# Performance work log

Measured on AMD Instinct MI355X. Metric: run time of the kernel, lower is better.

The kernel has to match this reference:

```python
import jax, jax.numpy as jnp
import numpy as np

N_NODES = 100000   # total atoms in the batched graph
N_EDGES = 1600000  # bonds (directed), avg degree 16
N_GRAPHS = 2000    # molecules in the batch
D_IN, D_H, D_OUT = 600, 300, 2  # 600 = embedding_dim(150) * 4


def setup_inputs() -> dict:
    key = jax.random.key(0)
    ks = jax.random.split(key, 8)
    node_feats = jax.random.normal(ks[0], (N_NODES, D_IN), dtype=jnp.float32)
    W1 = jax.random.normal(ks[1], (D_IN, D_H), dtype=jnp.float32) * (1.0 / np.sqrt(D_IN))
    b1 = jnp.zeros((D_H,), dtype=jnp.float32)
    W2 = jax.random.normal(ks[2], (D_H, D_H), dtype=jnp.float32) * (1.0 / np.sqrt(D_H))
    b2 = jnp.zeros((D_H,), dtype=jnp.float32)
    Wfc = jax.random.normal(ks[3], (D_H, D_OUT), dtype=jnp.float32) * (1.0 / np.sqrt(D_H))
    bfc = jnp.zeros((D_OUT,), dtype=jnp.float32)
    src = jax.random.randint(ks[4], (N_EDGES,), 0, N_NODES, dtype=jnp.int32).astype(jnp.int64)
    dst = jax.random.randint(ks[5], (N_EDGES,), 0, N_NODES, dtype=jnp.int32).astype(jnp.int64)
    graph_id = jnp.sort(jax.random.randint(ks[6], (N_NODES,), 0, N_GRAPHS, dtype=jnp.int32)).astype(jnp.int64)
    return {"node_feats": node_feats, "W1": W1, "b1": b1, "W2": W2, "b2": b2,
            "Wfc": Wfc, "bfc": bfc, "src": src, "dst": dst, "graph_id": graph_id}


def _gcn_layer(x, W, b, src, dst, inv_sqrt_out, inv_sqrt_in):
    # DGL GraphConv (norm='both'): h_i = d_i^{-1/2} * sum_{j->i} d_j^{-1/2} (x_j W) + b
    # weight applied before aggregation (in_feats >= out_feats path), math identical either way.
    h = x @ W                                  # [N, d_out]
    m = h * inv_sqrt_out[:, None]              # scale by src out-degree^{-1/2}
    agg = jax.ops.segment_sum(m[src], dst, num_segments=N_NODES)  # [N, d_out]
    return agg * inv_sqrt_in[:, None] + b


def reference(node_feats, W1, b1, W2, b2, Wfc, bfc, src, dst, graph_id):
    ones_e = jnp.ones((src.shape[0],), dtype=node_feats.dtype)
    deg_out = jax.ops.segment_sum(ones_e, src, num_segments=N_NODES)
    deg_in = jax.ops.segment_sum(ones_e, dst, num_segments=N_NODES)
    inv_sqrt_out = jnp.where(deg_out > 0, jax.lax.rsqrt(jnp.maximum(deg_out, 1.0)), 0.0)
    inv_sqrt_in = jnp.where(deg_in > 0, jax.lax.rsqrt(jnp.maximum(deg_in, 1.0)), 0.0)

    h = jax.nn.relu(_gcn_layer(node_feats, W1, b1, src, dst, inv_sqrt_out, inv_sqrt_in))
    h = jax.nn.relu(_gcn_layer(h, W2, b2, src, dst, inv_sqrt_out, inv_sqrt_in))
    p = jax.nn.softmax(h @ Wfc + bfc, axis=-1)  # [N, 2] per-node class probs

    # per-graph mean pooling (unbatch + mean over each graph's nodes)
    pooled_sum = jax.ops.segment_sum(p, graph_id, num_segments=N_GRAPHS)
    counts = jax.ops.segment_sum(jnp.ones((N_NODES,), dtype=p.dtype), graph_id, num_segments=N_GRAPHS)
    return pooled_sum / jnp.maximum(counts, 1.0)[:, None]  # [G, 2]
```

## Files before the change

### kernel.cpp

```cpp
#include <hip/hip_runtime.h>
#include <hip/hip_bf16.h>

#define N_NODES 100000
#define N_EDGES 1600000
#define N_GRAPHS 2000
#define D_IN 600
#define D_H 300
#define D_OUT 2

#define NPAD 320
#define K1PAD 640
#define K2PAD 320
#define MPAD 100096

typedef __bf16 bf16;
typedef __bf16 bf16x8 __attribute__((ext_vector_type(8)));
typedef float f32x4 __attribute__((ext_vector_type(4)));

__device__ __forceinline__ void gload16(const void* g, void* l) {
    __builtin_amdgcn_global_load_lds(
        (const __attribute__((address_space(1))) unsigned int*)g,
        (__attribute__((address_space(3))) unsigned int*)l, 16, 0, 0);
}

__global__ __launch_bounds__(256) void count_deg(const int* __restrict__ src,
                                                 const int* __restrict__ dst,
                                                 int* __restrict__ deg_out,
                                                 int* __restrict__ deg_in) {
    int e = blockIdx.x * blockDim.x + threadIdx.x;
    if (e < N_EDGES) {
        atomicAdd(&deg_out[src[e]], 1);
        atomicAdd(&deg_in[dst[e]], 1);
    }
}

__global__ __launch_bounds__(256) void block_sum(const int* __restrict__ deg_in,
                                                 int* __restrict__ bsum) {
    __shared__ int s[256];
    int i = blockIdx.x * 256 + threadIdx.x;
    s[threadIdx.x] = (i < N_NODES) ? deg_in[i] : 0;
    __syncthreads();
    for (int off = 128; off; off >>= 1) {
        if (threadIdx.x < off) s[threadIdx.x] += s[threadIdx.x + off];
        __syncthreads();
    }
    if (threadIdx.x == 0) bsum[blockIdx.x] = s[0];
}

__global__ void scan_serial(const int* __restrict__ bsum, int* __restrict__ boff, int nb) {
    if (threadIdx.x == 0 && blockIdx.x == 0) {
        int run = 0;
        for (int i = 0; i < nb; ++i) { boff[i] = run; run += bsum[i]; }
    }
}

__global__ __launch_bounds__(256) void node_offsets(const int* __restrict__ deg_in,
                                                    const int* __restrict__ deg_out,
                                                    const int* __restrict__ boff,
                                                    int* __restrict__ row_start,
                                                    int* __restrict__ cursor,
                                                    float* __restrict__ inv_in,
                                                    float* __restrict__ inv_out) {
    __shared__ int s[256];
    int i = blockIdx.x * 256 + threadIdx.x;
    int d = (i < N_NODES) ? deg_in[i] : 0;
    s[threadIdx.x] = d;
    __syncthreads();
    for (int off = 1; off < 256; off <<= 1) {
        int v = 0;
        if (threadIdx.x >= off) v = s[threadIdx.x - off];
        __syncthreads();
        if (threadIdx.x >= off) s[threadIdx.x] += v;
        __syncthreads();
    }
    if (i < N_NODES) {
        int excl = s[threadIdx.x] - d;
        int rs = boff[blockIdx.x] + excl;
        row_start[i] = rs;
        cursor[i] = rs;
        int di = deg_in[i];
        int dout = deg_out[i];
        inv_in[i]  = (di   > 0) ? rsqrtf((float)di)   : 0.0f;
        inv_out[i] = (dout > 0) ? rsqrtf((float)dout) : 0.0f;
    }
}

__global__ __launch_bounds__(256) void fill_csr(const int* __restrict__ src,
                                                const int* __restrict__ dst,
                                                int* __restrict__ cursor,
                                                int* __restrict__ adj) {
    int e = blockIdx.x * blockDim.x + threadIdx.x;
    if (e < N_EDGES) {
        int pos = atomicAdd(&cursor[dst[e]], 1);
        adj[pos] = src[e];
    }
}

__global__ __launch_bounds__(256) void conv_x(const float* __restrict__ x, bf16* __restrict__ xb) {
    size_t idx = (size_t)blockIdx.x * 256 + threadIdx.x;
    size_t r = idx / (K1PAD / 8);
    int c8 = (int)(idx % (K1PAD / 8)) * 8;
    if (r >= MPAD) return;
    bf16x8 v = {};
    if (r < N_NODES && c8 < D_IN) {
        const float* p = x + r * D_IN + c8;
        float4 f0 = *(const float4*)p;
        float4 f1 = *(const float4*)(p + 4);
        v[0] = (bf16)f0.x; v[1] = (bf16)f0.y; v[2] = (bf16)f0.z; v[3] = (bf16)f0.w;
        v[4] = (bf16)f1.x; v[5] = (bf16)f1.y; v[6] = (bf16)f1.z; v[7] = (bf16)f1.w;
    }
    *(bf16x8*)(xb + r * K1PAD + c8) = v;
}

__global__ __launch_bounds__(256) void conv_bt(const float* __restrict__ W, bf16* __restrict__ Bt,
                                               int K, int N, int Kpad) {
    int idx = blockIdx.x * 256 + threadIdx.x;
    int k = idx % Kpad;
    int n = idx / Kpad;
    if (n >= NPAD) return;
    bf16 v = (bf16)0.0f;
    if (k < K && n < N) v = (bf16)W[(size_t)k * N + n];
    Bt[(size_t)n * Kpad + k] = v;
}

__global__ __launch_bounds__(256) void prep_small(const float* __restrict__ b1,
                                                  const float* __restrict__ b2,
                                                  const float* __restrict__ Wfc,
                                                  float* __restrict__ b1p,
                                                  float* __restrict__ b2p,
                                                  float* __restrict__ wfcp) {
    int i = blockIdx.x * 256 + threadIdx.x;
    if (i < NPAD) {
        b1p[i] = (i < D_H) ? b1[i] : 0.f;
        b2p[i] = (i < D_H) ? b2[i] : 0.f;
    }
    if (i < NPAD * 2) {
        wfcp[i] = (i < D_H * 2) ? Wfc[i] : 0.f;
    }
}

__global__ __launch_bounds__(512) void mfma_gemm(const bf16* __restrict__ A,
                                                 const bf16* __restrict__ Bt,
                                                 const float* __restrict__ rowscale,
                                                 bf16* __restrict__ C,
                                                 int M, int Kpad) {
    __shared__ bf16 As[128 * 64];
    __shared__ bf16 Bs[320 * 64];
    const int tid = threadIdx.x;
    const int lane = tid & 63;
    const int wid = tid >> 6;
    const int wr = wid >> 2;
    const int wc = wid & 3;
    const int blockRow = blockIdx.x * 128;
    const size_t rowBytes = (size_t)Kpad * 2;

    f32x4 acc[4][5] = {};

    const int nK = Kpad >> 6;
    for (int t = 0; t < nK; ++t) {
        const size_t kByte = (size_t)t * 128;
#pragma unroll
        for (int c = 0; c < 2; ++c) {
            int o = c * 8192 + tid * 16;
            int row = o >> 7;
            int slot = (o >> 4) & 7;
            int srcs = slot ^ (row & 7);
            const char* g = (const char*)A + (size_t)(blockRow + row) * rowBytes + kByte + srcs * 16;
            gload16(g, (char*)As + o);
        }
#pragma unroll
        for (int c = 0; c < 5; ++c) {
            int o = c * 8192 + tid * 16;
            int row = o >> 7;
            int slot = (o >> 4) & 7;
            int srcs = slot ^ (row & 7);
            const char* g = (const char*)Bt + (size_t)row * rowBytes + kByte + srcs * 16;
            gload16(g, (char*)Bs + o);
        }
        __syncthreads();
#pragma unroll
        for (int kk = 0; kk < 2; ++kk) {
            int slot = kk * 4 + (lane >> 4);
            bf16x8 af[4], bfr[5];
#pragma unroll
            for (int mi = 0; mi < 4; ++mi) {
                int row = wr * 64 + mi * 16 + (lane & 15);
                int addr = row * 128 + ((slot ^ (row & 7)) << 4);
                af[mi] = *(const bf16x8*)((const char*)As + addr);
            }
#pragma unroll
            for (int ni = 0; ni < 5; ++ni) {
                int row = wc * 80 + ni * 16 + (lane & 15);
                int addr = row * 128 + ((slot ^ (row & 7)) << 4);
                bfr[ni] = *(const bf16x8*)((const char*)Bs + addr);
            }
#pragma unroll
            for (int mi = 0; mi < 4; ++mi)
#pragma unroll
                for (int ni = 0; ni < 5; ++ni)
                    acc[mi][ni] = __builtin_amdgcn_mfma_f32_16x16x32_bf16(af[mi], bfr[ni], acc[mi][ni], 0, 0, 0);
        }
        __syncthreads();
    }
#pragma unroll
    for (int mi = 0; mi < 4; ++mi) {
#pragma unroll
        for (int i = 0; i < 4; ++i) {
            int gr = blockRow + wr * 64 + mi * 16 + ((lane >> 4) << 2) + i;
            if (gr >= M) continue;
            float sc = rowscale[gr];
#pragma unroll
            for (int ni = 0; ni < 5; ++ni) {
                int gc = wc * 80 + ni * 16 + (lane & 15);
                C[(size_t)gr * NPAD + gc] = (bf16)(acc[mi][ni][i] * sc);
            }
        }
    }
}

__device__ __forceinline__ void gather8(const bf16* __restrict__ m,
                                        const int* __restrict__ adj,
                                        int s, int d, int c, float acc[8]) {
    int e = 0;
    for (; e + 8 <= d; e += 8) {
        bf16x8 v0 = *(const bf16x8*)(m + (size_t)adj[s + e + 0] * NPAD + c);
        bf16x8 v1 = *(const bf16x8*)(m + (size_t)adj[s + e + 1] * NPAD + c);
        bf16x8 v2 = *(const bf16x8*)(m + (size_t)adj[s + e + 2] * NPAD + c);
        bf16x8 v3 = *(const bf16x8*)(m + (size_t)adj[s + e + 3] * NPAD + c);
        bf16x8 v4 = *(const bf16x8*)(m + (size_t)adj[s + e + 4] * NPAD + c);
        bf16x8 v5 = *(const bf16x8*)(m + (size_t)adj[s + e + 5] * NPAD + c);
        bf16x8 v6 = *(const bf16x8*)(m + (size_t)adj[s + e + 6] * NPAD + c);
        bf16x8 v7 = *(const bf16x8*)(m + (size_t)adj[s + e + 7] * NPAD + c);
#pragma unroll
        for (int q = 0; q < 8; ++q)
            acc[q] += ((float)v0[q] + (float)v1[q]) + ((float)v2[q] + (float)v3[q]) +
                      ((float)v4[q] + (float)v5[q]) + ((float)v6[q] + (float)v7[q]);
    }
    if (e + 4 <= d) {
        bf16x8 v0 = *(const bf16x8*)(m + (size_t)adj[s + e + 0] * NPAD + c);
        bf16x8 v1 = *(const bf16x8*)(m + (size_t)adj[s + e + 1] * NPAD + c);
        bf16x8 v2 = *(const bf16x8*)(m + (size_t)adj[s + e + 2] * NPAD + c);
        bf16x8 v3 = *(const bf16x8*)(m + (size_t)adj[s + e + 3] * NPAD + c);
#pragma unroll
        for (int q = 0; q < 8; ++q)
            acc[q] += ((float)v0[q] + (float)v1[q]) + ((float)v2[q] + (float)v3[q]);
        e += 4;
    }
    for (; e < d; ++e) {
        bf16x8 v = *(const bf16x8*)(m + (size_t)adj[s + e] * NPAD + c);
#pragma unroll
        for (int q = 0; q < 8; ++q) acc[q] += (float)v[q];
    }
}

__global__ __launch_bounds__(256) void aggregate_bf16(const bf16* __restrict__ m,
                                                      const int* __restrict__ row_start,
                                                      const int* __restrict__ deg_in,
                                                      const int* __restrict__ adj,
                                                      const float* __restrict__ inv_in,
                                                      const float* __restrict__ biasp,
                                                      bf16* __restrict__ h) {
    int node = (int)((blockIdx.x * (size_t)blockDim.x + threadIdx.x) >> 6);
    int lane = threadIdx.x & 63;
    if (node >= N_NODES) return;
    if (lane >= 40) return;
    int s = row_start[node];
    int d = deg_in[node];
    int c = lane * 8;
    float acc[8] = {};
    gather8(m, adj, s, d, c, acc);
    float sc = inv_in[node];
    float4 bq0 = *(const float4*)(biasp + c);
    float4 bq1 = *(const float4*)(biasp + c + 4);
    float bv[8] = {bq0.x, bq0.y, bq0.z, bq0.w, bq1.x, bq1.y, bq1.z, bq1.w};
    bf16x8 o;
#pragma unroll
    for (int q = 0; q < 8; ++q) o[q] = (bf16)fmaxf(acc[q] * sc + bv[q], 0.f);
    *(bf16x8*)(h + (size_t)node * NPAD + c) = o;
}

__global__ __launch_bounds__(256) void agg2_fc_pool(const bf16* __restrict__ m,
                                                    const int* __restrict__ row_start,
                                                    const int* __restrict__ deg_in,
                                                    const int* __restrict__ adj,
                                                    const float* __restrict__ inv_in,
                                                    const float* __restrict__ biasp,
                                                    const float* __restrict__ wfcp,
                                                    const float* __restrict__ bfc,
                                                    const int* __restrict__ gid,
                                                    float* __restrict__ pooled,
                                                    int* __restrict__ gcount) {
    int node = (int)((blockIdx.x * (size_t)blockDim.x + threadIdx.x) >> 6);
    int lane = threadIdx.x & 63;
    if (node >= N_NODES) return;
    float z0 = 0.f, z1 = 0.f;
    if (lane < 40) {
        int s = row_start[node];
        int d = deg_in[node];
        int c = lane * 8;
        float acc[8] = {};
        gather8(m, adj, s, d, c, acc);
        float sc = inv_in[node];
        float4 bq0 = *(const float4*)(biasp + c);
        float4 bq1 = *(const float4*)(biasp + c + 4);
        float bv[8] = {bq0.x, bq0.y, bq0.z, bq0.w, bq1.x, bq1.y, bq1.z, bq1.w};
        float4 w0 = *(const float4*)(wfcp + c * 2);
        float4 w1 = *(const float4*)(wfcp + c * 2 + 4);
        float4 w2 = *(const float4*)(wfcp + c * 2 + 8);
        float4 w3 = *(const float4*)(wfcp + c * 2 + 12);
        float wz0[8] = {w0.x, w0.z, w1.x, w1.z, w2.x, w2.z, w3.x, w3.z};
        float wz1[8] = {w0.y, w0.w, w1.y, w1.w, w2.y, w2.w, w3.y, w3.w};
#pragma unroll
        for (int q = 0; q < 8; ++q) {
            float hq = fmaxf(acc[q] * sc + bv[q], 0.f);
            z0 += hq * wz0[q];
            z1 += hq * wz1[q];
        }
    }
    for (int off = 32; off; off >>= 1) {
        z0 += __shfl_down(z0, off);
        z1 += __shfl_down(z1, off);
    }
    if (lane == 0) {
        float s0 = z0 + bfc[0], s1 = z1 + bfc[1];
        float mx = fmaxf(s0, s1);
        float e0 = __expf(s0 - mx), e1 = __expf(s1 - mx);
        float inv = 1.f / (e0 + e1);
        int g = gid[node];
        atomicAdd(&pooled[g * 2 + 0], e0 * inv);
        atomicAdd(&pooled[g * 2 + 1], e1 * inv);
        atomicAdd(&gcount[g], 1);
    }
}

__global__ __launch_bounds__(256) void finalize(const float* __restrict__ pooled,
                                                const int* __restrict__ gcount,
                                                float* __restrict__ out) {
    int i = blockIdx.x * blockDim.x + threadIdx.x;
    if (i < N_GRAPHS * 2) {
        int g = i >> 1;
        float c = (float)max(gcount[g], 1);
        out[i] = pooled[i] / c;
    }
}

extern "C" void kernel_launch(void* const* d_in, const int* in_sizes, int n_in,
                              void* d_out, int out_size, void* d_ws, size_t ws_size,
                              hipStream_t stream) {
    const float* x   = (const float*)d_in[0];
    const float* W1  = (const float*)d_in[1];
    const float* b1  = (const float*)d_in[2];
    const float* W2  = (const float*)d_in[3];
    const float* b2  = (const float*)d_in[4];
    const float* Wfc = (const float*)d_in[5];
    const float* bfc = (const float*)d_in[6];
    const int* src   = (const int*)d_in[7];
    const int* dst   = (const int*)d_in[8];
    const int* gid   = (const int*)d_in[9];

    char* ws = (char*)d_ws;
    size_t off = 0;
    auto alloc = [&](size_t bytes) -> void* {
        void* p = ws + off;
        off = (off + bytes + 255) & ~(size_t)255;
        return p;
    };
    bf16* x_bf   = (bf16*)alloc((size_t)MPAD * K1PAD * 2);
    bf16* h_bf   = (bf16*)alloc((size_t)MPAD * NPAD * 2);
    bf16* m_bf   = (bf16*)alloc((size_t)N_NODES * NPAD * 2);
    bf16* B1t    = (bf16*)alloc((size_t)NPAD * K1PAD * 2);
    bf16* B2t    = (bf16*)alloc((size_t)NPAD * K2PAD * 2);
    int*   adj      = (int*)alloc((size_t)N_EDGES * 4);
    int*   row_st   = (int*)alloc((size_t)N_NODES * 4);
    int*   cursor   = (int*)alloc((size_t)N_NODES * 4);
    int*   deg_in   = (int*)alloc((size_t)N_NODES * 4);
    int*   deg_out  = (int*)alloc((size_t)N_NODES * 4);
    float* inv_in   = (float*)alloc((size_t)N_NODES * 4);
    float* inv_out  = (float*)alloc((size_t)N_NODES * 4);
    const int NB = (N_NODES + 255) / 256;
    int*   bsum     = (int*)alloc((size_t)NB * 4);
    int*   boff     = (int*)alloc((size_t)NB * 4);
    float* pooled   = (float*)alloc((size_t)N_GRAPHS * 2 * 4);
    int*   gcount   = (int*)alloc((size_t)N_GRAPHS * 4);
    float* b1p      = (float*)alloc((size_t)NPAD * 4);
    float* b2p      = (float*)alloc((size_t)NPAD * 4);
    float* wfcp     = (float*)alloc((size_t)NPAD * 2 * 4);

    hipMemsetAsync(deg_in, 0, (size_t)N_NODES * 4, stream);
    hipMemsetAsync(deg_out, 0, (size_t)N_NODES * 4, stream);
    hipMemsetAsync(pooled, 0, (size_t)N_GRAPHS * 2 * 4, stream);
    hipMemsetAsync(gcount, 0, (size_t)N_GRAPHS * 4, stream);

    count_deg<<<(N_EDGES + 255) / 256, 256, 0, stream>>>(src, dst, deg_out, deg_in);
    block_sum<<<NB, 256, 0, stream>>>(deg_in, bsum);
    scan_serial<<<1, 64, 0, stream>>>(bsum, boff, NB);
    node_offsets<<<NB, 256, 0, stream>>>(deg_in, deg_out, boff, row_st, cursor, inv_in, inv_out);
    fill_csr<<<(N_EDGES + 255) / 256, 256, 0, stream>>>(src, dst, cursor, adj);

    conv_x<<<(MPAD * (K1PAD / 8) + 255) / 256, 256, 0, stream>>>(x, x_bf);
    conv_bt<<<(NPAD * K1PAD + 255) / 256, 256, 0, stream>>>(W1, B1t, D_IN, D_H, K1PAD);
    conv_bt<<<(NPAD * K2PAD + 255) / 256, 256, 0, stream>>>(W2, B2t, D_H, D_H, K2PAD);
    prep_small<<<3, 256, 0, stream>>>(b1, b2, Wfc, b1p, b2p, wfcp);

    mfma_gemm<<<MPAD / 128, 512, 0, stream>>>(x_bf, B1t, inv_out, m_bf, N_NODES, K1PAD);
    aggregate_bf16<<<(N_NODES * 64 + 255) / 256, 256, 0, stream>>>(m_bf, row_st, deg_in, adj, inv_in, b1p, h_bf);
    mfma_gemm<<<MPAD / 128, 512, 0, stream>>>(h_bf, B2t, inv_out, m_bf, N_NODES, K2PAD);
    agg2_fc_pool<<<(N_NODES * 64 + 255) / 256, 256, 0, stream>>>(m_bf, row_st, deg_in, adj, inv_in, b2p,
                                                                 wfcp, bfc, gid, pooled, gcount);
    finalize<<<(N_GRAPHS * 2 + 255) / 256, 256, 0, stream>>>(pooled, gcount, (float*)d_out);
}
```

Before: 827.8 us.

## Fuse fp32-to-bf16 input conversion into first GEMM and pack aggregation threads densely

Removes the separate conv_x pass and its padded bf16 copy of node_feats. The first GEMM now reads fp32 rows directly, converts them in registers and writes them swizzled into LDS, which cuts one full read-write round trip of a 240MB tensor. Both aggregation kernels now map 40 threads per node with no idle lanes instead of 64-lane wavefronts with 24 idle. The second kernel reduces its FC logits through LDS atomics instead of wave shuffles. The trade-off is that the GEMM's A loads are now synchronous register loads rather than async global-to-LDS loads, and node work can straddle wavefront boundaries.

```diff
diff --git a/kernel.cpp b/kernel.cpp
--- a/kernel.cpp
+++ b/kernel.cpp
@@ -96,22 +96,6 @@
     }
 }
 
-__global__ __launch_bounds__(256) void conv_x(const float* __restrict__ x, bf16* __restrict__ xb) {
-    size_t idx = (size_t)blockIdx.x * 256 + threadIdx.x;
-    size_t r = idx / (K1PAD / 8);
-    int c8 = (int)(idx % (K1PAD / 8)) * 8;
-    if (r >= MPAD) return;
-    bf16x8 v = {};
-    if (r < N_NODES && c8 < D_IN) {
-        const float* p = x + r * D_IN + c8;
-        float4 f0 = *(const float4*)p;
-        float4 f1 = *(const float4*)(p + 4);
-        v[0] = (bf16)f0.x; v[1] = (bf16)f0.y; v[2] = (bf16)f0.z; v[3] = (bf16)f0.w;
-        v[4] = (bf16)f1.x; v[5] = (bf16)f1.y; v[6] = (bf16)f1.z; v[7] = (bf16)f1.w;
-    }
-    *(bf16x8*)(xb + r * K1PAD + c8) = v;
-}
-
 __global__ __launch_bounds__(256) void conv_bt(const float* __restrict__ W, bf16* __restrict__ Bt,
                                                int K, int N, int Kpad) {
     int idx = blockIdx.x * 256 + threadIdx.x;
@@ -136,6 +120,93 @@
     }
     if (i < NPAD * 2) {
         wfcp[i] = (i < D_H * 2) ? Wfc[i] : 0.f;
+    }
+}
+
+__global__ __launch_bounds__(512) void mfma_gemm_f32A(const float* __restrict__ A,
+                                                      const bf16* __restrict__ Bt,
+                                                      const float* __restrict__ rowscale,
+                                                      bf16* __restrict__ C) {
+    __shared__ bf16 As[128 * 64];
+    __shared__ bf16 Bs[320 * 64];
+    const int tid = threadIdx.x;
+    const int lane = tid & 63;
+    const int wid = tid >> 6;
+    const int wr = wid >> 2;
+    const int wc = wid & 3;
+    const int blockRow = blockIdx.x * 128;
+    const size_t rowBytesB = (size_t)K1PAD * 2;
+
+    f32x4 acc[4][5] = {};
+
+    const int nK = K1PAD >> 6;
+    for (int t = 0; t < nK; ++t) {
+        const size_t kByte = (size_t)t * 128;
+#pragma unroll
+        for (int c = 0; c < 2; ++c) {
+            int o = c * 8192 + tid * 16;
+            int row = o >> 7;
+            int slot = (o >> 4) & 7;
+            int gr = blockRow + row;
+            int k = t * 64 + slot * 8;
+            bf16x8 v = {};
+            if (gr < N_NODES && k < D_IN) {
+                const float* p = A + (size_t)gr * D_IN + k;
+                float4 f0 = *(const float4*)p;
+                float4 f1 = *(const float4*)(p + 4);
+                v[0] = (bf16)f0.x; v[1] = (bf16)f0.y; v[2] = (bf16)f0.z; v[3] = (bf16)f0.w;
+                v[4] = (bf16)f1.x; v[5] = (bf16)f1.y; v[6] = (bf16)f1.z; v[7] = (bf16)f1.w;
+            }
+            int waddr = row * 128 + ((slot ^ (row & 7)) << 4);
+            *(bf16x8*)((char*)As + waddr) = v;
+        }
+#pragma unroll
+        for (int c = 0; c < 5; ++c) {
+            int o = c * 8192 + tid * 16;
+            int row = o >> 7;
+            int slot = (o >> 4) & 7;
+            int srcs = slot ^ (row & 7);
+            const char* g = (const char*)Bt + (size_t)row * rowBytesB + kByte + srcs * 16;
+            gload16(g, (char*)Bs + o);
+        }
+        __syncthreads();
+#pragma unroll
+        for (int kk = 0; kk < 2; ++kk) {
+            int slot = kk * 4 + (lane >> 4);
+            bf16x8 af[4], bfr[5];
+#pragma unroll
+            for (int mi = 0; mi < 4; ++mi) {
+                int row = wr * 64 + mi * 16 + (lane & 15);
+                int addr = row * 128 + ((slot ^ (row & 7)) << 4);
+                af[mi] = *(const bf16x8*)((const char*)As + addr);
+            }
+#pragma unroll
+            for (int ni = 0; ni < 5; ++ni) {
+                int row = wc * 80 + ni * 16 + (lane & 15);
+                int addr = row * 128 + ((slot ^ (row & 7)) << 4);
+                bfr[ni] = *(const bf16x8*)((const char*)Bs + addr);
+            }
+#pragma unroll
+            for (int mi = 0; mi < 4; ++mi)
+#pragma unroll
+                for (int ni = 0; ni < 5; ++ni)
+                    acc[mi][ni] = __builtin_amdgcn_mfma_f32_16x16x32_bf16(af[mi], bfr[ni], acc[mi][ni], 0, 0, 0);
+        }
+        __syncthreads();
+    }
+#pragma unroll
+    for (int mi = 0; mi < 4; ++mi) {
+#pragma unroll
+        for (int i = 0; i < 4; ++i) {
+            int gr = blockRow + wr * 64 + mi * 16 + ((lane >> 4) << 2) + i;
+            if (gr >= N_NODES) continue;
+            float sc = rowscale[gr];
+#pragma unroll
+            for (int ni = 0; ni < 5; ++ni) {
+                int gc = wc * 80 + ni * 16 + (lane & 15);
+                C[(size_t)gr * NPAD + gc] = (bf16)(acc[mi][ni][i] * sc);
+            }
+        }
     }
 }
 
@@ -253,20 +324,20 @@
     }
 }
 
-__global__ __launch_bounds__(256) void aggregate_bf16(const bf16* __restrict__ m,
+__global__ __launch_bounds__(320) void aggregate_flat(const bf16* __restrict__ m,
                                                       const int* __restrict__ row_start,
                                                       const int* __restrict__ deg_in,
                                                       const int* __restrict__ adj,
                                                       const float* __restrict__ inv_in,
                                                       const float* __restrict__ biasp,
                                                       bf16* __restrict__ h) {
-    int node = (int)((blockIdx.x * (size_t)blockDim.x + threadIdx.x) >> 6);
-    int lane = threadIdx.x & 63;
+    int t = blockIdx.x * 320 + threadIdx.x;
+    int node = t / 40;
+    int chunk = t % 40;
     if (node >= N_NODES) return;
-    if (lane >= 40) return;
     int s = row_start[node];
     int d = deg_in[node];
-    int c = lane * 8;
+    int c = chunk * 8;
     float acc[8] = {};
     gather8(m, adj, s, d, c, acc);
     float sc = inv_in[node];
@@ -279,7 +350,7 @@
     *(bf16x8*)(h + (size_t)node * NPAD + c) = o;
 }
 
-__global__ __launch_bounds__(256) void agg2_fc_pool(const bf16* __restrict__ m,
+__global__ __launch_bounds__(320) void agg2_fc_pool(const bf16* __restrict__ m,
                                                     const int* __restrict__ row_start,
                                                     const int* __restrict__ deg_in,
                                                     const int* __restrict__ adj,
@@ -290,14 +361,17 @@
                                                     const int* __restrict__ gid,
                                                     float* __restrict__ pooled,
                                                     int* __restrict__ gcount) {
-    int node = (int)((blockIdx.x * (size_t)blockDim.x + threadIdx.x) >> 6);
-    int lane = threadIdx.x & 63;
-    if (node >= N_NODES) return;
+    __shared__ float red0[8], red1[8];
+    int nl = threadIdx.x / 40;
+    int chunk = threadIdx.x % 40;
+    int node = blockIdx.x * 8 + nl;
+    if (threadIdx.x < 8) { red0[threadIdx.x] = 0.f; red1[threadIdx.x] = 0.f; }
+    __syncthreads();
     float z0 = 0.f, z1 = 0.f;
-    if (lane < 40) {
+    if (node < N_NODES) {
         int s = row_start[node];
         int d = deg_in[node];
-        int c = lane * 8;
+        int c = chunk * 8;
         float acc[8] = {};
         gather8(m, adj, s, d, c, acc);
         float sc = inv_in[node];
@@ -316,13 +390,12 @@
             z0 += hq * wz0[q];
             z1 += hq * wz1[q];
         }
-    }
-    for (int off = 32; off; off >>= 1) {
-        z0 += __shfl_down(z0, off);
-        z1 += __shfl_down(z1, off);
-    }
-    if (lane == 0) {
-        float s0 = z0 + bfc[0], s1 = z1 + bfc[1];
+        atomicAdd(&red0[nl], z0);
+        atomicAdd(&red1[nl], z1);
+    }
+    __syncthreads();
+    if (chunk == 0 && node < N_NODES) {
+        float s0 = red0[nl] + bfc[0], s1 = red1[nl] + bfc[1];
         float mx = fmaxf(s0, s1);
         float e0 = __expf(s0 - mx), e1 = __expf(s1 - mx);
         float inv = 1.f / (e0 + e1);
@@ -365,7 +438,6 @@
         off = (off + bytes + 255) & ~(size_t)255;
         return p;
     };
-    bf16* x_bf   = (bf16*)alloc((size_t)MPAD * K1PAD * 2);
     bf16* h_bf   = (bf16*)alloc((size_t)MPAD * NPAD * 2);
     bf16* m_bf   = (bf16*)alloc((size_t)N_NODES * NPAD * 2);
     bf16* B1t    = (bf16*)alloc((size_t)NPAD * K1PAD * 2);
@@ -397,15 +469,14 @@
     node_offsets<<<NB, 256, 0, stream>>>(deg_in, deg_out, boff, row_st, cursor, inv_in, inv_out);
     fill_csr<<<(N_EDGES + 255) / 256, 256, 0, stream>>>(src, dst, cursor, adj);
 
-    conv_x<<<(MPAD * (K1PAD / 8) + 255) / 256, 256, 0, stream>>>(x, x_bf);
     conv_bt<<<(NPAD * K1PAD + 255) / 256, 256, 0, stream>>>(W1, B1t, D_IN, D_H, K1PAD);
     conv_bt<<<(NPAD * K2PAD + 255) / 256, 256, 0, stream>>>(W2, B2t, D_H, D_H, K2PAD);
     prep_small<<<3, 256, 0, stream>>>(b1, b2, Wfc, b1p, b2p, wfcp);
 
-    mfma_gemm<<<MPAD / 128, 512, 0, stream>>>(x_bf, B1t, inv_out, m_bf, N_NODES, K1PAD);
-    aggregate_bf16<<<(N_NODES * 64 + 255) / 256, 256, 0, stream>>>(m_bf, row_st, deg_in, adj, inv_in, b1p, h_bf);
+    mfma_gemm_f32A<<<MPAD / 128, 512, 0, stream>>>(x, B1t, inv_out, m_bf);
+    aggregate_flat<<<(N_NODES * 40 + 319) / 320, 320, 0, stream>>>(m_bf, row_st, deg_in, adj, inv_in, b1p, h_bf);
     mfma_gemm<<<MPAD / 128, 512, 0, stream>>>(h_bf, B2t, inv_out, m_bf, N_NODES, K2PAD);
-    agg2_fc_pool<<<(N_NODES * 64 + 255) / 256, 256, 0, stream>>>(m_bf, row_st, deg_in, adj, inv_in, b2p,
-                                                                 wfcp, bfc, gid, pooled, gcount);
+    agg2_fc_pool<<<(N_NODES + 7) / 8, 320, 0, stream>>>(m_bf, row_st, deg_in, adj, inv_in, b2p,
+                                                        wfcp, bfc, gid, pooled, gcount);
     finalize<<<(N_GRAPHS * 2 + 255) / 256, 256, 0, stream>>>(pooled, gcount, (float*)d_out);
 }
```

Result: slower. 900.9 us (+8.8%).
